# Kernel optimization log

Hardware: AMD Instinct MI355X
Metric: run time of the kernel (lower is better)

The kernel has to match this reference:

```python
import jax, jax.numpy as jnp
import numpy as np

B, I, H = 4096, 1024, 1024


def setup_inputs() -> dict:
    key = jax.random.key(0)
    ks = jax.random.split(key, 7)
    s = 0.1  # matches uniform(-0.1, 0.1) init scale loosely
    return {
        "input": jax.random.normal(ks[0], (B, I), jnp.float32),
        "h_t": jax.random.normal(ks[1], (B, H), jnp.float32),
        "c_t": jax.random.normal(ks[2], (B, H), jnp.float32),
        "w_i": jax.random.uniform(ks[3], (I, 4 * H), jnp.float32, -s, s),
        "w_h": jax.random.uniform(ks[4], (H, 4 * H), jnp.float32, -s, s),
        "b_i": jax.random.uniform(ks[5], (4 * H,), jnp.float32, -s, s),
        "b_h": jax.random.uniform(ks[6], (4 * H,), jnp.float32, -s, s),
    }


def reference(input, h_t, c_t, w_i, w_h, b_i, b_h):
    # ifgo: [B, 4H] = x @ w_i + h @ w_h + b_i + b_h
    ifgo = input @ w_i + h_t @ w_h + (b_i + b_h)
    i, f, g, o = jnp.split(ifgo, 4, axis=1)
    i = jax.nn.sigmoid(i)
    f = jax.nn.sigmoid(f)
    g = jnp.tanh(g)
    o = jax.nn.sigmoid(o)
    c_new = f * c_t + i * g
    h_new = o * jnp.tanh(c_new)
    return (h_new, c_new)
```

## Files before the change

### kernel.cpp

```cpp
#include <hip/hip_runtime.h>
#include <stdint.h>

typedef __attribute__((ext_vector_type(8))) short short8;
typedef __attribute__((ext_vector_type(4))) float floatx4;

__device__ inline unsigned short f2bf(float x) {
  union { float f; unsigned int u; } v; v.f = x;
  unsigned int r = v.u + 0x7FFFu + ((v.u >> 16) & 1u);
  return (unsigned short)(r >> 16);
}

__global__ void pack_A(const float* __restrict__ x, const float* __restrict__ h,
                       unsigned short* __restrict__ A) {
  int gid = blockIdx.x * 256 + threadIdx.x;
  int row = gid >> 7;
  int kc  = (gid & 127) << 4;
  const float* src = (kc < 1024) ? (x + (size_t)row * 1024 + kc)
                                 : (h + (size_t)row * 1024 + (kc - 1024));
  const float4* s = (const float4*)src;
  float4 a = s[0], b = s[1], c = s[2], d = s[3];
  uint4 o0, o1;
  o0.x = f2bf(a.x) | ((unsigned)f2bf(a.y) << 16);
  o0.y = f2bf(a.z) | ((unsigned)f2bf(a.w) << 16);
  o0.z = f2bf(b.x) | ((unsigned)f2bf(b.y) << 16);
  o0.w = f2bf(b.z) | ((unsigned)f2bf(b.w) << 16);
  o1.x = f2bf(c.x) | ((unsigned)f2bf(c.y) << 16);
  o1.y = f2bf(c.z) | ((unsigned)f2bf(c.w) << 16);
  o1.z = f2bf(d.x) | ((unsigned)f2bf(d.y) << 16);
  o1.w = f2bf(d.z) | ((unsigned)f2bf(d.w) << 16);
  unsigned short* dst = A + (size_t)row * 2048 + kc;
  *(uint4*)dst = o0;
  *(uint4*)(dst + 8) = o1;
}

__global__ void pack_W(const float* __restrict__ wi, const float* __restrict__ wh,
                       unsigned short* __restrict__ Wt) {
  __shared__ float tile[64][129];
  int b2 = blockIdx.x;
  int kt = b2 & 31;
  int nt = b2 >> 5;
  int k0 = kt << 6, n0 = nt << 7;
  const float* src = (k0 < 1024) ? (wi + (size_t)k0 * 4096)
                                 : (wh + (size_t)(k0 - 1024) * 4096);
  int t = threadIdx.x;
  int c4 = (t & 31) << 2, rr = t >> 5;
#pragma unroll
  for (int p = 0; p < 8; ++p) {
    int kk = rr + p * 8;
    float4 v = *(const float4*)(src + (size_t)kk * 4096 + n0 + c4);
    tile[kk][c4 + 0] = v.x; tile[kk][c4 + 1] = v.y;
    tile[kk][c4 + 2] = v.z; tile[kk][c4 + 3] = v.w;
  }
  __syncthreads();
  int k8 = (t & 7) << 3, nn = t >> 3;
#pragma unroll
  for (int p = 0; p < 4; ++p) {
    int nl = nn + p * 32;
    int n = n0 + nl;
    int hh = n & 1023, g = n >> 10;
    int R = ((hh >> 5) << 7) + (((hh >> 4) & 1) << 6) + (g << 4) + (hh & 15);
    uint4 o;
    o.x = f2bf(tile[k8 + 0][nl]) | ((unsigned)f2bf(tile[k8 + 1][nl]) << 16);
    o.y = f2bf(tile[k8 + 2][nl]) | ((unsigned)f2bf(tile[k8 + 3][nl]) << 16);
    o.z = f2bf(tile[k8 + 4][nl]) | ((unsigned)f2bf(tile[k8 + 5][nl]) << 16);
    o.w = f2bf(tile[k8 + 6][nl]) | ((unsigned)f2bf(tile[k8 + 7][nl]) << 16);
    *(uint4*)(Wt + (size_t)R * 2048 + k0 + k8) = o;
  }
}

__device__ inline void gl_lds16(const void* g, void* l) {
  __builtin_amdgcn_global_load_lds(
      (const __attribute__((address_space(1))) void*)g,
      (__attribute__((address_space(3))) void*)l, 16, 0, 0);
}

__device__ inline float sigm(float x)  { return 1.0f / (1.0f + __expf(-x)); }
__device__ inline float tanhx(float x) { return 2.0f / (1.0f + __expf(-2.0f * x)) - 1.0f; }

__global__ void __launch_bounds__(256, 2) gemm_lstm(
    const unsigned short* __restrict__ A,
    const unsigned short* __restrict__ Bt,
    const float* __restrict__ ct,
    const float* __restrict__ bi,
    const float* __restrict__ bh,
    float* __restrict__ out) {
  constexpr int K = 2048;
  __shared__ char AsB[256 * 128];
  __shared__ char BsB[128 * 128];
  const int tid  = threadIdx.x;
  const int lane = tid & 63;
  const int wave = tid >> 6;
  const int wm = wave >> 1, wn = wave & 1;

  const int bid = blockIdx.x;
  const int g  = bid & 7;
  const int s  = bid >> 3;
  const int bx = (g << 2) + (s & 3);
  const int by = s >> 2;
  const int m0 = by << 8;
  const int n0 = bx << 7;
  const int h0 = bx << 5;

  const int er = (lane >> 4) << 2;
  const int ec = lane & 15;
  const int h  = h0 + (wn << 4) + ec;
  float bias[4];
#pragma unroll
  for (int j = 0; j < 4; ++j) bias[j] = bi[j * 1024 + h] + bh[j * 1024 + h];

  const int sr = tid >> 3;
  const int cs = ((tid & 7) ^ (sr & 7)) << 4;
  const unsigned voff = (unsigned)sr * 4096u + (unsigned)cs;
  const char* aBase = (const char*)A  + (size_t)m0 * 4096;
  const char* bBase = (const char*)Bt + (size_t)n0 * 4096;
  char* aD = AsB + tid * 16;
  char* bD = BsB + tid * 16;

  floatx4 acc[8][4] = {};
  const int rA = (wm << 7) + (lane & 15);
  const int rB = (wn << 6) + (lane & 15);
  const int keyc = lane & 7;
  const int kq   = lane >> 4;
  const char* aF0 = AsB + rA * 128 + ((kq ^ keyc) << 4);
  const char* aF1 = AsB + rA * 128 + (((4 + kq) ^ keyc) << 4);
  const char* bF0 = BsB + rB * 128 + ((kq ^ keyc) << 4);
  const char* bF1 = BsB + rB * 128 + (((4 + kq) ^ keyc) << 4);

  for (int ks = 0; ks < K; ks += 64) {
    const char* aIt = aBase + ks * 2;
    const char* bIt = bBase + ks * 2;
#pragma unroll
    for (int p = 0; p < 8; ++p) gl_lds16(aIt + p * 131072 + voff, aD + p * 4096);
#pragma unroll
    for (int p = 0; p < 4; ++p) gl_lds16(bIt + p * 131072 + voff, bD + p * 4096);
    __syncthreads();
    {
      short8 af[8], bfr[4];
#pragma unroll
      for (int f = 0; f < 8; ++f) af[f] = *(const short8*)(aF0 + f * 2048);
#pragma unroll
      for (int f = 0; f < 4; ++f) bfr[f] = *(const short8*)(bF0 + f * 2048);
#pragma unroll
      for (int i = 0; i < 8; ++i)
#pragma unroll
        for (int j = 0; j < 4; ++j)
          acc[i][j] = __builtin_amdgcn_mfma_f32_16x16x32_bf16(af[i], bfr[j], acc[i][j], 0, 0, 0);
    }
    {
      short8 af[8], bfr[4];
#pragma unroll
      for (int f = 0; f < 8; ++f) af[f] = *(const short8*)(aF1 + f * 2048);
#pragma unroll
      for (int f = 0; f < 4; ++f) bfr[f] = *(const short8*)(bF1 + f * 2048);
#pragma unroll
      for (int i = 0; i < 8; ++i)
#pragma unroll
        for (int j = 0; j < 4; ++j)
          acc[i][j] = __builtin_amdgcn_mfma_f32_16x16x32_bf16(af[i], bfr[j], acc[i][j], 0, 0, 0);
    }
    __syncthreads();
  }

  float cv[8][4];
#pragma unroll
  for (int i = 0; i < 8; ++i)
#pragma unroll
    for (int rg = 0; rg < 4; ++rg) {
      int row = m0 + (wm << 7) + i * 16 + er + rg;
      cv[i][rg] = ct[(size_t)row * 1024 + h];
    }
#pragma unroll
  for (int i = 0; i < 8; ++i) {
#pragma unroll
    for (int rg = 0; rg < 4; ++rg) {
      int row = m0 + (wm << 7) + i * 16 + er + rg;
      size_t o = (size_t)row * 1024 + h;
      float iv = sigm(acc[i][0][rg] + bias[0]);
      float fv = sigm(acc[i][1][rg] + bias[1]);
      float gv = tanhx(acc[i][2][rg] + bias[2]);
      float ov = sigm(acc[i][3][rg] + bias[3]);
      float cn = fv * cv[i][rg] + iv * gv;
      out[o] = ov * tanhx(cn);
      out[4194304 + o] = cn;
    }
  }
}

extern "C" void kernel_launch(void* const* d_in, const int* in_sizes, int n_in,
                              void* d_out, int out_size, void* d_ws, size_t ws_size,
                              hipStream_t stream) {
  const float* x  = (const float*)d_in[0];
  const float* ht = (const float*)d_in[1];
  const float* ct = (const float*)d_in[2];
  const float* wi = (const float*)d_in[3];
  const float* wh = (const float*)d_in[4];
  const float* bi = (const float*)d_in[5];
  const float* bh = (const float*)d_in[6];
  float* out = (float*)d_out;

  char* ws = (char*)d_ws;
  unsigned short* Abf = (unsigned short*)ws;
  unsigned short* Wbf = (unsigned short*)(ws + (16u << 20));

  pack_A<<<2048, 256, 0, stream>>>(x, ht, Abf);
  pack_W<<<1024, 256, 0, stream>>>(wi, wh, Wbf);
  gemm_lstm<<<512, 256, 0, stream>>>(Abf, Wbf, ct, bi, bh, out);
}
```

Baseline: 197.6 us.

## Double-buffer LDS with 256x256 tiles, 8 waves, and staggered prefetch pipeline

The GEMM moves from a 256x128 tile with 4 waves to a 256x256 tile with 8 waves. Global-to-LDS loads now go into ping-pong A/B buffers, so the next K-slice is fetched while MFMAs run on the current one, with partial vmcnt waits and s_setprio around the MFMA bursts. This targets the exposed load latency and the paired full barriers of the single-buffered loop, and the larger tile raises operand reuse. In exchange it needs 128KB of LDS per block, launches half as many blocks (256), and relies on fragile manual waitcnt and barrier ordering.

```diff
diff --git a/kernel.cpp b/kernel.cpp
--- a/kernel.cpp
+++ b/kernel.cpp
@@ -77,90 +77,115 @@
 __device__ inline float sigm(float x)  { return 1.0f / (1.0f + __expf(-x)); }
 __device__ inline float tanhx(float x) { return 2.0f / (1.0f + __expf(-2.0f * x)) - 1.0f; }
 
-__global__ void __launch_bounds__(256, 2) gemm_lstm(
+#define MFMA_BF16 __builtin_amdgcn_mfma_f32_16x16x32_bf16
+
+#define STAGE4(SRC, DSTARR)                                            \
+  do {                                                                 \
+    _Pragma("unroll")                                                  \
+    for (int p = 0; p < 4; ++p)                                        \
+      gl_lds16((SRC) + rOff + (size_t)p * 262144,                      \
+               (char*)(DSTARR) + tid * 16 + p * 8192);                 \
+  } while (0)
+
+#define TILE(CA, CB, NA, AN, BN)                                              \
+  {                                                                           \
+    const char* aS = aBase + (size_t)(((AN) & 31) << 7);                      \
+    const char* bS = bBase + (size_t)(((BN) & 31) << 7);                      \
+    const char* pa_ = (const char*)(CA) + aRowOff;                            \
+    const char* pb_ = (const char*)(CB) + bRowOff;                            \
+    short8 a0[8], b0[4];                                                      \
+    _Pragma("unroll")                                                         \
+    for (int j = 0; j < 4; ++j) b0[j] = *(const short8*)(pb_ + j * 2048 + c0);\
+    _Pragma("unroll")                                                         \
+    for (int i = 0; i < 8; ++i) a0[i] = *(const short8*)(pa_ + i * 2048 + c0);\
+    STAGE4(aS, NA);                                                           \
+    asm volatile("s_waitcnt lgkmcnt(0)" ::: "memory");                        \
+    __builtin_amdgcn_s_setprio(1);                                            \
+    _Pragma("unroll")                                                         \
+    for (int i = 0; i < 8; ++i)                                               \
+      _Pragma("unroll")                                                       \
+      for (int j = 0; j < 4; ++j)                                             \
+        acc[i][j] = MFMA_BF16(a0[i], b0[j], acc[i][j], 0, 0, 0);              \
+    __builtin_amdgcn_s_setprio(0);                                            \
+    short8 a1[8], b1[4];                                                      \
+    _Pragma("unroll")                                                         \
+    for (int j = 0; j < 4; ++j) b1[j] = *(const short8*)(pb_ + j * 2048 + c1);\
+    _Pragma("unroll")                                                         \
+    for (int i = 0; i < 8; ++i) a1[i] = *(const short8*)(pa_ + i * 2048 + c1);\
+    asm volatile("s_waitcnt lgkmcnt(0)" ::: "memory");                        \
+    __builtin_amdgcn_s_barrier();                                             \
+    STAGE4(bS, CB);                                                           \
+    __builtin_amdgcn_s_setprio(1);                                            \
+    _Pragma("unroll")                                                         \
+    for (int i = 0; i < 8; ++i)                                               \
+      _Pragma("unroll")                                                       \
+      for (int j = 0; j < 4; ++j)                                             \
+        acc[i][j] = MFMA_BF16(a1[i], b1[j], acc[i][j], 0, 0, 0);              \
+    __builtin_amdgcn_s_setprio(0);                                            \
+    asm volatile("s_waitcnt vmcnt(4)" ::: "memory");                          \
+    __builtin_amdgcn_s_barrier();                                             \
+  }
+
+__global__ void __launch_bounds__(512, 2) gemm_lstm(
     const unsigned short* __restrict__ A,
     const unsigned short* __restrict__ Bt,
     const float* __restrict__ ct,
     const float* __restrict__ bi,
     const float* __restrict__ bh,
     float* __restrict__ out) {
-  constexpr int K = 2048;
-  __shared__ char AsB[256 * 128];
-  __shared__ char BsB[128 * 128];
+  __shared__ __align__(16) char A0[32768];
+  __shared__ __align__(16) char A1[32768];
+  __shared__ __align__(16) char B0[32768];
+  __shared__ __align__(16) char B1[32768];
+
   const int tid  = threadIdx.x;
   const int lane = tid & 63;
   const int wave = tid >> 6;
-  const int wm = wave >> 1, wn = wave & 1;
+  const int wm = wave >> 2;
+  const int wn = wave & 3;
 
   const int bid = blockIdx.x;
-  const int g  = bid & 7;
-  const int s  = bid >> 3;
-  const int bx = (g << 2) + (s & 3);
-  const int by = s >> 2;
+  const int gx = bid & 7;
+  const int sx = bid >> 3;
+  const int bx = (gx << 1) + (sx & 1);
+  const int by = sx >> 1;
   const int m0 = by << 8;
-  const int n0 = bx << 7;
-  const int h0 = bx << 5;
+
+  const int ec = lane & 15;
+  const int h  = (bx << 6) + ((wn >> 1) << 5) + ((wn & 1) << 4) + ec;
+  float bias[4];
+#pragma unroll
+  for (int j = 0; j < 4; ++j) bias[j] = bi[j * 1024 + h] + bh[j * 1024 + h];
+
+  const int sr = tid >> 3;
+  const unsigned swz = (unsigned)(((tid & 7) ^ (sr & 7)) << 4);
+  const size_t rOff = (size_t)sr * 4096 + swz;
+  const char* aBase = (const char*)A  + (size_t)m0 * 4096;
+  const char* bBase = (const char*)Bt + (size_t)(bx << 8) * 4096;
+
+  const int lr  = lane & 15;
+  const int kq  = lane >> 4;
+  const int key = lane & 7;
+  const int c0  = (kq ^ key) << 4;
+  const int c1  = ((4 + kq) ^ key) << 4;
+  const int aRowOff = ((wm << 7) + lr) * 128;
+  const int bRowOff = ((wn << 6) + lr) * 128;
+
+  floatx4 acc[8][4] = {};
+
+  STAGE4(bBase, B0);
+  STAGE4(aBase, A0);
+  STAGE4(bBase + 128, B1);
+  asm volatile("s_waitcnt vmcnt(4)" ::: "memory");
+  __builtin_amdgcn_s_barrier();
+
+  for (int it = 0; it < 16; ++it) {
+    const int t = it << 1;
+    TILE(A0, B0, A1, t + 1, t + 2);
+    TILE(A1, B1, A0, t + 2, t + 3);
+  }
 
   const int er = (lane >> 4) << 2;
-  const int ec = lane & 15;
-  const int h  = h0 + (wn << 4) + ec;
-  float bias[4];
-#pragma unroll
-  for (int j = 0; j < 4; ++j) bias[j] = bi[j * 1024 + h] + bh[j * 1024 + h];
-
-  const int sr = tid >> 3;
-  const int cs = ((tid & 7) ^ (sr & 7)) << 4;
-  const unsigned voff = (unsigned)sr * 4096u + (unsigned)cs;
-  const char* aBase = (const char*)A  + (size_t)m0 * 4096;
-  const char* bBase = (const char*)Bt + (size_t)n0 * 4096;
-  char* aD = AsB + tid * 16;
-  char* bD = BsB + tid * 16;
-
-  floatx4 acc[8][4] = {};
-  const int rA = (wm << 7) + (lane & 15);
-  const int rB = (wn << 6) + (lane & 15);
-  const int keyc = lane & 7;
-  const int kq   = lane >> 4;
-  const char* aF0 = AsB + rA * 128 + ((kq ^ keyc) << 4);
-  const char* aF1 = AsB + rA * 128 + (((4 + kq) ^ keyc) << 4);
-  const char* bF0 = BsB + rB * 128 + ((kq ^ keyc) << 4);
-  const char* bF1 = BsB + rB * 128 + (((4 + kq) ^ keyc) << 4);
-
-  for (int ks = 0; ks < K; ks += 64) {
-    const char* aIt = aBase + ks * 2;
-    const char* bIt = bBase + ks * 2;
-#pragma unroll
-    for (int p = 0; p < 8; ++p) gl_lds16(aIt + p * 131072 + voff, aD + p * 4096);
-#pragma unroll
-    for (int p = 0; p < 4; ++p) gl_lds16(bIt + p * 131072 + voff, bD + p * 4096);
-    __syncthreads();
-    {
-      short8 af[8], bfr[4];
-#pragma unroll
-      for (int f = 0; f < 8; ++f) af[f] = *(const short8*)(aF0 + f * 2048);
-#pragma unroll
-      for (int f = 0; f < 4; ++f) bfr[f] = *(const short8*)(bF0 + f * 2048);
-#pragma unroll
-      for (int i = 0; i < 8; ++i)
-#pragma unroll
-        for (int j = 0; j < 4; ++j)
-          acc[i][j] = __builtin_amdgcn_mfma_f32_16x16x32_bf16(af[i], bfr[j], acc[i][j], 0, 0, 0);
-    }
-    {
-      short8 af[8], bfr[4];
-#pragma unroll
-      for (int f = 0; f < 8; ++f) af[f] = *(const short8*)(aF1 + f * 2048);
-#pragma unroll
-      for (int f = 0; f < 4; ++f) bfr[f] = *(const short8*)(bF1 + f * 2048);
-#pragma unroll
-      for (int i = 0; i < 8; ++i)
-#pragma unroll
-        for (int j = 0; j < 4; ++j)
-          acc[i][j] = __builtin_amdgcn_mfma_f32_16x16x32_bf16(af[i], bfr[j], acc[i][j], 0, 0, 0);
-    }
-    __syncthreads();
-  }
-
   float cv[8][4];
 #pragma unroll
   for (int i = 0; i < 8; ++i)
@@ -204,5 +229,5 @@
 
   pack_A<<<2048, 256, 0, stream>>>(x, ht, Abf);
   pack_W<<<1024, 256, 0, stream>>>(wi, wh, Wbf);
-  gemm_lstm<<<512, 256, 0, stream>>>(Abf, Wbf, ct, bi, bh, out);
-}
+  gemm_lstm<<<256, 512, 0, stream>>>(Abf, Wbf, ct, bi, bh, out);
+}
```

Measured after the change: 199.6 us. About the same (+1.0%).
